# Kernel optimization log

Hardware: AMD Instinct MI355X
Metric: run time of the kernel (lower is better)

Reference implementation:

```python
import jax, jax.numpy as jnp
import numpy as np

HEADS = 8
DH = 64      # dim_head
KS = 3       # kernel_size (padding=1, stride=1, dilation=1 -> same-resolution window)


def _unfold3x3(t):
    # t: [b, c, H, W] -> patches [b, c, 9, H, W], window positions in row-major
    # order, matching torch F.unfold channel ordering (c major, kernel pos minor).
    b, c, H, W = t.shape
    tp = jnp.pad(t, ((0, 0), (0, 0), (1, 1), (1, 1)))
    return jnp.stack([tp[:, :, i:i + H, j:j + W]
                      for i in range(KS) for j in range(KS)], axis=2)


def setup_inputs() -> dict:
    key = jax.random.key(0)
    k0, k1, k2, k3 = jax.random.split(key, 4)
    b, c, H, W = 16, 256, 32, 32
    inner = HEADS * DH  # 512
    x = jax.random.normal(k0, (b, c, H, W), jnp.float32)
    Wq = jax.random.normal(k1, (inner, c), jnp.float32) * 0.02      # to_q 1x1 conv
    Wkv = jax.random.normal(k2, (2 * inner, c), jnp.float32) * 0.02  # to_kv 1x1 conv (k=1)
    Wo = jax.random.normal(k3, (c, inner), jnp.float32) * 0.02       # to_out 1x1 conv
    bo = jnp.zeros((c,), jnp.float32)
    return {"x": x, "Wq": Wq, "Wkv": Wkv, "Wo": Wo, "bo": bo}


def reference(x, Wq, Wkv, Wo, bo):
    b, c, H, W = x.shape
    n = H * W
    w = KS * KS
    scale = DH ** -0.5

    # 1x1 convs as channel matmuls
    q = jnp.einsum('bcxy,oc->boxy', x, Wq)               # [b, h*d, H, W]
    q = q.reshape(b, HEADS, DH, n).transpose(0, 1, 3, 2)  # [b, h, n, d]
    kv = jnp.einsum('bcxy,oc->boxy', x, Wkv)
    k, v = jnp.split(kv, 2, axis=1)                       # each [b, h*d, H, W]

    def to_windows(t):
        p = _unfold3x3(t)                                  # [b, h*d, 9, H, W]
        return p.reshape(b, HEADS, DH, w, n).transpose(0, 1, 4, 3, 2)  # [b,h,n,w,d]

    k = to_windows(k)
    v = to_windows(v)

    # einsum over d directly == original repeat(q over w) + elementwise*sum
    dots = jnp.einsum('bhnd,bhnwd->bhnw', q, k) * scale
    attn = jax.nn.softmax(dots, axis=-1)
    out = jnp.einsum('bhnw,bhnwd->bhnd', attn, v)          # [b, h, n, d]
    out = out.transpose(0, 1, 3, 2).reshape(b, HEADS * DH, H, W)
    out = jnp.einsum('bcxy,oc->boxy', out, Wo) + bo[None, :, None, None]
    return (out, attn)
```

## Files before the change

### kernel.cpp

```cpp
#include <hip/hip_runtime.h>

#define NPIX   1024
#define BATCH  16
#define CIN    256
#define NQKV   1536
#define INNER  512
#define HEADS  8
#define DH     64

typedef __attribute__((ext_vector_type(8))) short short8;
typedef __attribute__((ext_vector_type(4))) float f32x4;

__device__ __forceinline__ ushort f2b(float f) {
    union { float f; unsigned u; } v; v.f = f;
    unsigned r = v.u + 0x7fffu + ((v.u >> 16) & 1u);
    return (ushort)(r >> 16);
}
__device__ __forceinline__ float b2f(ushort u) {
    union { float f; unsigned u; } v; v.u = ((unsigned)u) << 16; return v.f;
}
__device__ __forceinline__ void async16(const void* g, void* l) {
    __builtin_amdgcn_global_load_lds((const __attribute__((address_space(1))) void*)g,
                                     (__attribute__((address_space(3))) void*)l, 16, 0, 0);
}

__global__ __launch_bounds__(256) void prep_x(const float* __restrict__ x,
                                              ushort* __restrict__ xT) {
    __shared__ float tile[32][33];
    const int b  = blockIdx.z;
    const int p0 = blockIdx.x * 32;
    const int c0 = blockIdx.y * 32;
    const int tx = threadIdx.x, ty = threadIdx.y;
#pragma unroll
    for (int i = 0; i < 4; i++) {
        int c = ty + i * 8;
        tile[c][tx] = x[(b * CIN + c0 + c) * NPIX + p0 + tx];
    }
    __syncthreads();
#pragma unroll
    for (int i = 0; i < 4; i++) {
        int p = ty + i * 8;
        xT[(b * NPIX + p0 + p) * CIN + c0 + tx] = f2b(tile[tx][p]);
    }
}

__global__ __launch_bounds__(256) void prep_w(const float* __restrict__ Wq,
        const float* __restrict__ Wkv, const float* __restrict__ Wo,
        ushort* __restrict__ Wqkv_b, ushort* __restrict__ Wob) {
    int i = blockIdx.x * 256 + threadIdx.x;
    if (i < NQKV * CIN)
        Wqkv_b[i] = f2b(i < INNER * CIN ? Wq[i] : Wkv[i - INNER * CIN]);
    int j = i - NQKV * CIN;
    if (j >= 0 && j < CIN * INNER)
        Wob[j] = f2b(Wo[j]);
}

__global__ __launch_bounds__(256) void gemm_qkv(const ushort* __restrict__ xT,
        const ushort* __restrict__ Wb, ushort* __restrict__ qkv) {
    __shared__ ushort Ws[128][32];
    __shared__ ushort Xs[128][32];
    const int m0 = blockIdx.x * 128;
    const int n0 = blockIdx.y * 128;
    const int t    = threadIdx.x;
    const int wave = t >> 6, lane = t & 63;
    const int wo = (wave & 1) * 64, wp = (wave >> 1) * 64;
    const int lrow = lane & 15, loct = lane >> 4;

    const int srow = t >> 2;
    const int skb  = (t & 3) * 8;
    const ushort* gA = Wb + (n0 + srow) * CIN + skb;
    const ushort* gB = xT + (m0 + srow) * CIN + skb;
    ushort* ldsA0 = &Ws[wave * 16][0];
    ushort* ldsA1 = &Ws[64 + wave * 16][0];
    ushort* ldsB0 = &Xs[wave * 16][0];
    ushort* ldsB1 = &Xs[64 + wave * 16][0];

    f32x4 acc[4][4];
#pragma unroll
    for (int i = 0; i < 4; i++)
#pragma unroll
        for (int j = 0; j < 4; j++) acc[i][j] = (f32x4){0.f, 0.f, 0.f, 0.f};

    for (int c0 = 0; c0 < CIN; c0 += 32) {
        async16(gA + c0, ldsA0);
        async16(gA + 64 * CIN + c0, ldsA1);
        async16(gB + c0, ldsB0);
        async16(gB + 64 * CIN + c0, ldsB1);
        __syncthreads();
        short8 a[4], bb[4];
#pragma unroll
        for (int i = 0; i < 4; i++)
            a[i] = *reinterpret_cast<const short8*>(&Ws[wo + i * 16 + lrow][loct * 8]);
#pragma unroll
        for (int j = 0; j < 4; j++)
            bb[j] = *reinterpret_cast<const short8*>(&Xs[wp + j * 16 + lrow][loct * 8]);
#pragma unroll
        for (int i = 0; i < 4; i++)
#pragma unroll
            for (int j = 0; j < 4; j++)
                acc[i][j] = __builtin_amdgcn_mfma_f32_16x16x32_bf16(a[i], bb[j], acc[i][j], 0, 0, 0);
        __syncthreads();
    }
#pragma unroll
    for (int i = 0; i < 4; i++)
#pragma unroll
        for (int j = 0; j < 4; j++) {
            int gm = m0 + wp + j * 16 + lrow;
            int go = n0 + wo + i * 16 + loct * 4;
            ushort4 pk = make_ushort4(f2b(acc[i][j].x), f2b(acc[i][j].y),
                                      f2b(acc[i][j].z), f2b(acc[i][j].w));
            *reinterpret_cast<ushort4*>(&qkv[gm * NQKV + go]) = pk;
        }
}

__global__ __launch_bounds__(256) void attn_kernel(const ushort* __restrict__ qkv,
        ushort* __restrict__ po, float* __restrict__ attn_out) {
    const int m    = blockIdx.x * 4 + (threadIdx.x >> 6);
    const int lane = threadIdx.x & 63;
    const int h = lane >> 3, sub = lane & 7;
    const int b = m >> 10;
    const int p = m & 1023;
    const int py = p >> 5, px = p & 31;
    const int hd8 = h * DH + sub * 8;

    short8 qv = *reinterpret_cast<const short8*>(&qkv[m * NQKV + hd8]);
    float qf[8];
#pragma unroll
    for (int j = 0; j < 8; j++) qf[j] = b2f((ushort)qv[j]);

    float dots[9];
    int   nb[9];
    bool  ok[9];
#pragma unroll
    for (int w = 0; w < 9; w++) {
        int dy = w / 3 - 1, dx = w % 3 - 1;
        int ny = py + dy, nx = px + dx;
        bool in = ((unsigned)ny < 32u) && ((unsigned)nx < 32u);
        ok[w] = in;
        int nm = b * NPIX + ny * 32 + nx;
        nb[w] = nm;
        float d = 0.f;
        if (in) {
            short8 kv8 = *reinterpret_cast<const short8*>(&qkv[nm * NQKV + 512 + hd8]);
#pragma unroll
            for (int j = 0; j < 8; j++) d = fmaf(qf[j], b2f((ushort)kv8[j]), d);
        }
        d += __shfl_xor(d, 1);
        d += __shfl_xor(d, 2);
        d += __shfl_xor(d, 4);
        dots[w] = d * 0.125f;
    }

    float mx = dots[0];
#pragma unroll
    for (int w = 1; w < 9; w++) mx = fmaxf(mx, dots[w]);
    float e[9], s = 0.f;
#pragma unroll
    for (int w = 0; w < 9; w++) { e[w] = __expf(dots[w] - mx); s += e[w]; }
    const float inv = 1.f / s;

    float o[8] = {};
#pragma unroll
    for (int w = 0; w < 9; w++) {
        if (ok[w]) {
            short8 vv = *reinterpret_cast<const short8*>(&qkv[nb[w] * NQKV + 1024 + hd8]);
            float pw = e[w] * inv;
#pragma unroll
            for (int j = 0; j < 8; j++) o[j] = fmaf(pw, b2f((ushort)vv[j]), o[j]);
        }
    }
    short8 r;
#pragma unroll
    for (int j = 0; j < 8; j++) r[j] = (short)f2b(o[j]);
    *reinterpret_cast<short8*>(&po[m * INNER + hd8]) = r;

    float* ab = &attn_out[((b * HEADS + h) * NPIX + p) * 9];
    ab[sub] = e[sub] * inv;
    if (sub == 0) ab[8] = e[8] * inv;
}

__global__ __launch_bounds__(256) void gemm_out(const ushort* __restrict__ po,
        const ushort* __restrict__ Wob, const float* __restrict__ bo,
        float* __restrict__ out) {
    __shared__ ushort As[128][32];
    __shared__ ushort Bs[128][32];
    const int m0 = blockIdx.x * 128;
    const int n0 = blockIdx.y * 128;
    const int t    = threadIdx.x;
    const int wave = t >> 6, lane = t & 63;
    const int wm = (wave >> 1) * 64, wn = (wave & 1) * 64;
    const int lrow = lane & 15, loct = lane >> 4;

    const int srow = t >> 2;
    const int skb  = (t & 3) * 8;
    const ushort* gA = po  + (m0 + srow) * INNER + skb;
    const ushort* gB = Wob + (n0 + srow) * INNER + skb;
    ushort* ldsA0 = &As[wave * 16][0];
    ushort* ldsA1 = &As[64 + wave * 16][0];
    ushort* ldsB0 = &Bs[wave * 16][0];
    ushort* ldsB1 = &Bs[64 + wave * 16][0];

    f32x4 acc[4][4];
#pragma unroll
    for (int i = 0; i < 4; i++)
#pragma unroll
        for (int j = 0; j < 4; j++) acc[i][j] = (f32x4){0.f, 0.f, 0.f, 0.f};

    for (int c0 = 0; c0 < INNER; c0 += 32) {
        async16(gA + c0, ldsA0);
        async16(gA + 64 * INNER + c0, ldsA1);
        async16(gB + c0, ldsB0);
        async16(gB + 64 * INNER + c0, ldsB1);
        __syncthreads();
        short8 a[4], bb[4];
#pragma unroll
        for (int i = 0; i < 4; i++)
            a[i] = *reinterpret_cast<const short8*>(&As[wm + i * 16 + lrow][loct * 8]);
#pragma unroll
        for (int j = 0; j < 4; j++)
            bb[j] = *reinterpret_cast<const short8*>(&Bs[wn + j * 16 + lrow][loct * 8]);
#pragma unroll
        for (int i = 0; i < 4; i++)
#pragma unroll
            for (int j = 0; j < 4; j++)
                acc[i][j] = __builtin_amdgcn_mfma_f32_16x16x32_bf16(a[i], bb[j], acc[i][j], 0, 0, 0);
        __syncthreads();
    }
    const int bb_ = m0 >> 10;
    const int p0  = m0 & 1023;
#pragma unroll
    for (int i = 0; i < 4; i++)
#pragma unroll
        for (int j = 0; j < 4; j++) {
            int o  = n0 + wn + j * 16 + lrow;
            int pp = p0 + wm + i * 16 + loct * 4;
            float bias = bo[o];
            float4 v = make_float4(acc[i][j].x + bias, acc[i][j].y + bias,
                                   acc[i][j].z + bias, acc[i][j].w + bias);
            *reinterpret_cast<float4*>(&out[(bb_ * CIN + o) * NPIX + pp]) = v;
        }
}

extern "C" void kernel_launch(void* const* d_in, const int* in_sizes, int n_in,
                              void* d_out, int out_size, void* d_ws, size_t ws_size,
                              hipStream_t stream) {
    const float* x   = (const float*)d_in[0];
    const float* Wq  = (const float*)d_in[1];
    const float* Wkv = (const float*)d_in[2];
    const float* Wo  = (const float*)d_in[3];
    const float* bo  = (const float*)d_in[4];

    float* out  = (float*)d_out;
    float* attn = out + BATCH * CIN * NPIX;

    ushort* xT     = (ushort*)d_ws;
    ushort* Wqkv_b = xT + 16384 * CIN;
    ushort* Wob    = Wqkv_b + NQKV * CIN;
    ushort* qkv    = Wob + CIN * INNER;
    ushort* po     = qkv + 16384 * NQKV;

    prep_x<<<dim3(32, 8, BATCH), dim3(32, 8), 0, stream>>>(x, xT);
    prep_w<<<2048, 256, 0, stream>>>(Wq, Wkv, Wo, Wqkv_b, Wob);

    gemm_qkv<<<dim3(128, 12), 256, 0, stream>>>(xT, Wqkv_b, qkv);

    attn_kernel<<<16384 / 4, 256, 0, stream>>>(qkv, po, attn);

    gemm_out<<<dim3(128, 2), 256, 0, stream>>>(po, Wob, bo, out);
}
```

Before: 139.8 us.

## Merge prep kernels, drop LDS staging in GEMMs, swizzle block order

Merges the x-transpose and weight-conversion kernels into one launch. Both GEMMs now load MFMA operands straight from global memory into registers instead of staging through LDS with barriers, and the k-loop is unrolled. Block indices in the GEMMs and the attention kernel are remapped so consecutive blocks are spread across the 8 XCDs for better L2 locality. The aim is to cut launch overhead and synchronisation, at the cost of more redundant global/L2 traffic because waves no longer share tiles through LDS.

```diff
diff --git a/kernel.cpp b/kernel.cpp
--- a/kernel.cpp
+++ b/kernel.cpp
@@ -19,61 +19,53 @@
 __device__ __forceinline__ float b2f(ushort u) {
     union { float f; unsigned u; } v; v.u = ((unsigned)u) << 16; return v.f;
 }
-__device__ __forceinline__ void async16(const void* g, void* l) {
-    __builtin_amdgcn_global_load_lds((const __attribute__((address_space(1))) void*)g,
-                                     (__attribute__((address_space(3))) void*)l, 16, 0, 0);
-}
-
-__global__ __launch_bounds__(256) void prep_x(const float* __restrict__ x,
-                                              ushort* __restrict__ xT) {
-    __shared__ float tile[32][33];
-    const int b  = blockIdx.z;
-    const int p0 = blockIdx.x * 32;
-    const int c0 = blockIdx.y * 32;
-    const int tx = threadIdx.x, ty = threadIdx.y;
-#pragma unroll
-    for (int i = 0; i < 4; i++) {
-        int c = ty + i * 8;
-        tile[c][tx] = x[(b * CIN + c0 + c) * NPIX + p0 + tx];
-    }
-    __syncthreads();
-#pragma unroll
-    for (int i = 0; i < 4; i++) {
-        int p = ty + i * 8;
-        xT[(b * NPIX + p0 + p) * CIN + c0 + tx] = f2b(tile[tx][p]);
-    }
-}
-
-__global__ __launch_bounds__(256) void prep_w(const float* __restrict__ Wq,
-        const float* __restrict__ Wkv, const float* __restrict__ Wo,
+
+__global__ __launch_bounds__(256) void prep_all(const float* __restrict__ x,
+        const float* __restrict__ Wq, const float* __restrict__ Wkv,
+        const float* __restrict__ Wo, ushort* __restrict__ xT,
         ushort* __restrict__ Wqkv_b, ushort* __restrict__ Wob) {
-    int i = blockIdx.x * 256 + threadIdx.x;
-    if (i < NQKV * CIN)
-        Wqkv_b[i] = f2b(i < INNER * CIN ? Wq[i] : Wkv[i - INNER * CIN]);
-    int j = i - NQKV * CIN;
-    if (j >= 0 && j < CIN * INNER)
-        Wob[j] = f2b(Wo[j]);
+    const int bid = blockIdx.x;
+    if (bid < 4096) {
+        __shared__ float tile[32][33];
+        const int b   = bid >> 8;
+        const int rem = bid & 255;
+        const int p0  = (rem & 31) * 32;
+        const int c0  = (rem >> 5) * 32;
+        const int tx = threadIdx.x & 31, ty = threadIdx.x >> 5;
+#pragma unroll
+        for (int i = 0; i < 4; i++) {
+            int c = ty + i * 8;
+            tile[c][tx] = x[(b * CIN + c0 + c) * NPIX + p0 + tx];
+        }
+        __syncthreads();
+#pragma unroll
+        for (int i = 0; i < 4; i++) {
+            int p = ty + i * 8;
+            xT[(b * NPIX + p0 + p) * CIN + c0 + tx] = f2b(tile[tx][p]);
+        }
+    } else {
+        int i = (bid - 4096) * 256 + threadIdx.x;
+        if (i < NQKV * CIN)
+            Wqkv_b[i] = f2b(i < INNER * CIN ? Wq[i] : Wkv[i - INNER * CIN]);
+        int j = i - NQKV * CIN;
+        if (j >= 0 && j < CIN * INNER)
+            Wob[j] = f2b(Wo[j]);
+    }
 }
 
 __global__ __launch_bounds__(256) void gemm_qkv(const ushort* __restrict__ xT,
         const ushort* __restrict__ Wb, ushort* __restrict__ qkv) {
-    __shared__ ushort Ws[128][32];
-    __shared__ ushort Xs[128][32];
-    const int m0 = blockIdx.x * 128;
-    const int n0 = blockIdx.y * 128;
+    const int bid = blockIdx.x;
+    const int swz = (bid & 7) * 192 + (bid >> 3);
+    const int m0  = (swz / 12) * 128;
+    const int n0  = (swz % 12) * 128;
     const int t    = threadIdx.x;
     const int wave = t >> 6, lane = t & 63;
     const int wo = (wave & 1) * 64, wp = (wave >> 1) * 64;
     const int lrow = lane & 15, loct = lane >> 4;
 
-    const int srow = t >> 2;
-    const int skb  = (t & 3) * 8;
-    const ushort* gA = Wb + (n0 + srow) * CIN + skb;
-    const ushort* gB = xT + (m0 + srow) * CIN + skb;
-    ushort* ldsA0 = &Ws[wave * 16][0];
-    ushort* ldsA1 = &Ws[64 + wave * 16][0];
-    ushort* ldsB0 = &Xs[wave * 16][0];
-    ushort* ldsB1 = &Xs[64 + wave * 16][0];
+    const ushort* aB = Wb + (n0 + wo + lrow) * CIN + loct * 8;
+    const ushort* bB = xT + (m0 + wp + lrow) * CIN + loct * 8;
 
     f32x4 acc[4][4];
 #pragma unroll
@@ -81,26 +73,22 @@
 #pragma unroll
         for (int j = 0; j < 4; j++) acc[i][j] = (f32x4){0.f, 0.f, 0.f, 0.f};
 
+#pragma unroll 4
     for (int c0 = 0; c0 < CIN; c0 += 32) {
-        async16(gA + c0, ldsA0);
-        async16(gA + 64 * CIN + c0, ldsA1);
-        async16(gB + c0, ldsB0);
-        async16(gB + 64 * CIN + c0, ldsB1);
-        __syncthreads();
         short8 a[4], bb[4];
 #pragma unroll
         for (int i = 0; i < 4; i++)
-            a[i] = *reinterpret_cast<const short8*>(&Ws[wo + i * 16 + lrow][loct * 8]);
+            a[i] = *reinterpret_cast<const short8*>(aB + i * 16 * CIN + c0);
 #pragma unroll
         for (int j = 0; j < 4; j++)
-            bb[j] = *reinterpret_cast<const short8*>(&Xs[wp + j * 16 + lrow][loct * 8]);
+            bb[j] = *reinterpret_cast<const short8*>(bB + j * 16 * CIN + c0);
 #pragma unroll
         for (int i = 0; i < 4; i++)
 #pragma unroll
             for (int j = 0; j < 4; j++)
                 acc[i][j] = __builtin_amdgcn_mfma_f32_16x16x32_bf16(a[i], bb[j], acc[i][j], 0, 0, 0);
-        __syncthreads();
-    }
+    }
+
 #pragma unroll
     for (int i = 0; i < 4; i++)
 #pragma unroll
@@ -115,7 +103,9 @@
 
 __global__ __launch_bounds__(256) void attn_kernel(const ushort* __restrict__ qkv,
         ushort* __restrict__ po, float* __restrict__ attn_out) {
-    const int m    = blockIdx.x * 4 + (threadIdx.x >> 6);
+    const int bid = blockIdx.x;
+    const int swz = (bid & 7) * 512 + (bid >> 3);
+    const int m    = swz * 4 + (threadIdx.x >> 6);
     const int lane = threadIdx.x & 63;
     const int h = lane >> 3, sub = lane & 7;
     const int b = m >> 10;
@@ -182,23 +172,17 @@
 __global__ __launch_bounds__(256) void gemm_out(const ushort* __restrict__ po,
         const ushort* __restrict__ Wob, const float* __restrict__ bo,
         float* __restrict__ out) {
-    __shared__ ushort As[128][32];
-    __shared__ ushort Bs[128][32];
-    const int m0 = blockIdx.x * 128;
-    const int n0 = blockIdx.y * 128;
+    const int bid = blockIdx.x;
+    const int swz = (bid & 7) * 32 + (bid >> 3);
+    const int m0  = (swz >> 1) * 128;
+    const int n0  = (swz & 1) * 128;
     const int t    = threadIdx.x;
     const int wave = t >> 6, lane = t & 63;
     const int wm = (wave >> 1) * 64, wn = (wave & 1) * 64;
     const int lrow = lane & 15, loct = lane >> 4;
 
-    const int srow = t >> 2;
-    const int skb  = (t & 3) * 8;
-    const ushort* gA = po  + (m0 + srow) * INNER + skb;
-    const ushort* gB = Wob + (n0 + srow) * INNER + skb;
-    ushort* ldsA0 = &As[wave * 16][0];
-    ushort* ldsA1 = &As[64 + wave * 16][0];
-    ushort* ldsB0 = &Bs[wave * 16][0];
-    ushort* ldsB1 = &Bs[64 + wave * 16][0];
+    const ushort* aB = po  + (m0 + wm + lrow) * INNER + loct * 8;
+    const ushort* bB = Wob + (n0 + wn + lrow) * INNER + loct * 8;
 
     f32x4 acc[4][4];
 #pragma unroll
@@ -206,26 +190,22 @@
 #pragma unroll
         for (int j = 0; j < 4; j++) acc[i][j] = (f32x4){0.f, 0.f, 0.f, 0.f};
 
+#pragma unroll 4
     for (int c0 = 0; c0 < INNER; c0 += 32) {
-        async16(gA + c0, ldsA0);
-        async16(gA + 64 * INNER + c0, ldsA1);
-        async16(gB + c0, ldsB0);
-        async16(gB + 64 * INNER + c0, ldsB1);
-        __syncthreads();
         short8 a[4], bb[4];
 #pragma unroll
         for (int i = 0; i < 4; i++)
-            a[i] = *reinterpret_cast<const short8*>(&As[wm + i * 16 + lrow][loct * 8]);
+            a[i] = *reinterpret_cast<const short8*>(aB + i * 16 * INNER + c0);
 #pragma unroll
         for (int j = 0; j < 4; j++)
-            bb[j] = *reinterpret_cast<const short8*>(&Bs[wn + j * 16 + lrow][loct * 8]);
+            bb[j] = *reinterpret_cast<const short8*>(bB + j * 16 * INNER + c0);
 #pragma unroll
         for (int i = 0; i < 4; i++)
 #pragma unroll
             for (int j = 0; j < 4; j++)
                 acc[i][j] = __builtin_amdgcn_mfma_f32_16x16x32_bf16(a[i], bb[j], acc[i][j], 0, 0, 0);
-        __syncthreads();
-    }
+    }
+
     const int bb_ = m0 >> 10;
     const int p0  = m0 & 1023;
 #pragma unroll
@@ -259,12 +239,11 @@
     ushort* qkv    = Wob + CIN * INNER;
     ushort* po     = qkv + 16384 * NQKV;
 
-    prep_x<<<dim3(32, 8, BATCH), dim3(32, 8), 0, stream>>>(x, xT);
-    prep_w<<<2048, 256, 0, stream>>>(Wq, Wkv, Wo, Wqkv_b, Wob);
-
-    gemm_qkv<<<dim3(128, 12), 256, 0, stream>>>(xT, Wqkv_b, qkv);
+    prep_all<<<6144, 256, 0, stream>>>(x, Wq, Wkv, Wo, xT, Wqkv_b, Wob);
+
+    gemm_qkv<<<1536, 256, 0, stream>>>(xT, Wqkv_b, qkv);
 
     attn_kernel<<<16384 / 4, 256, 0, stream>>>(qkv, po, attn);
 
-    gemm_out<<<dim3(128, 2), 256, 0, stream>>>(po, Wob, bo, out);
-}
+    gemm_out<<<256, 256, 0, stream>>>(po, Wob, bo, out);
+}
```

Result: slower. 171.1 us (+22.4%).
